# Kernel tuning notes

Hardware: AMD Instinct MI355X
Metric: run time of the kernel (lower is better)

Reference implementation:

```python
import jax, jax.numpy as jnp
import numpy as np

LEAKY_SLOPE = 0.2
DENSITY = 0.05


def setup_inputs() -> dict:
    key = jax.random.key(0)
    k1, k2, k3, k4, k5, k6 = jax.random.split(key, 6)
    N, F_in, F_out = 8192, 128, 64
    h = jax.random.normal(k1, (N, F_in), dtype=jnp.float32)
    # Linear(in, out, bias=False) weight is [out, in]
    W = jax.random.normal(k2, (F_out, F_in), dtype=jnp.float32) * (1.0 / np.sqrt(F_in))
    a_left = jax.random.normal(k3, (F_out,), dtype=jnp.float32) * 0.1
    a_right = jax.random.normal(k4, (F_out,), dtype=jnp.float32) * 0.1
    vals = jax.random.uniform(k5, (N, N), dtype=jnp.float32)
    keep = jax.random.uniform(k6, (N, N)) < DENSITY
    adj = jnp.where(keep, vals, 0.0)  # raw adjacency; self-loops added in reference
    return {"h": h, "W": W, "a_left": a_left, "a_right": a_right, "adj": adj}


def reference(h, W, a_left, a_right, adj):
    N = adj.shape[0]
    A = adj + jnp.eye(N, dtype=adj.dtype)          # A = adjacency + I (self-loops)
    mask = jnp.abs(A) > 0                          # valued-mask support
    Wh = h @ W.T                                   # [N, F_out]
    e_left = Wh @ a_left                           # [N]
    e_right = Wh @ a_right                         # [N]
    e = e_left[:, None] + e_right[None, :]         # [N, N] additive scores
    e = jnp.where(e >= 0, e, LEAKY_SLOPE * e)      # LeakyReLU(0.2)
    e = jnp.where(mask, e, -jnp.inf)               # masked_fill(mask==0, -inf)
    attention = jax.nn.softmax(e, axis=1) * A      # valued masking post-softmax
    # dropout p=0.0 -> identity (eval-mode reference)
    return attention @ Wh                          # [N, F_out]
```

## Files before the change

### kernel.cpp

```cpp
#include <hip/hip_runtime.h>
#include <hip/hip_bf16.h>
#include <hip/hip_fp16.h>

#define N    8192
#define FIN  128
#define FOUT 64
#define LEAKY 0.2f
#define CAP  640
#define LOG2E 1.44269504088896340736f

struct alignas(8) Ent { unsigned joff; float w; };

__global__ __launch_bounds__(256) void wh_eLR_kernel(
    const float* __restrict__ h, const float* __restrict__ Wm,
    const float* __restrict__ aL, const float* __restrict__ aR,
    __half* __restrict__ Whh, float* __restrict__ eL2, float* __restrict__ eR2)
{
    __shared__ float sW[FOUT][FIN + 1];
    __shared__ float sh[4][FIN];
    const int t = threadIdx.x;
    const int rbase = blockIdx.x * 4;

    for (int idx = t; idx < FOUT * FIN; idx += 256)
        sW[idx >> 7][idx & 127] = Wm[idx];
    for (int idx = t; idx < 4 * FIN; idx += 256)
        sh[idx >> 7][idx & 127] = h[(size_t)(rbase + (idx >> 7)) * FIN + (idx & 127)];
    __syncthreads();

    const int wv = t >> 6, f = t & 63;
    const int row = rbase + wv;
    float acc = 0.f;
    #pragma unroll 16
    for (int k = 0; k < FIN; ++k) acc += sh[wv][k] * sW[f][k];
    Whh[(size_t)row * FOUT + f] = __float2half_rn(acc);

    float vl = acc * aL[f];
    float vr = acc * aR[f];
    #pragma unroll
    for (int d = 32; d > 0; d >>= 1) {
        vl += __shfl_down(vl, d, 64);
        vr += __shfl_down(vr, d, 64);
    }
    if (f == 0) { eL2[row] = vl * LOG2E; eR2[row] = vr * LOG2E; }
}

__global__ __launch_bounds__(256) void gat_row_kernel(
    const float* __restrict__ adj, const __half* __restrict__ Whh,
    const float* __restrict__ eL2p, const float* __restrict__ eR2p,
    float* __restrict__ out)
{
    __shared__ Ent ent[4][CAP];
    const int t = threadIdx.x;
    const int wv = t >> 6;
    const int lane = t & 63;
    const int row = blockIdx.x * 4 + wv;

    const float el = eL2p[row];
    const float4* __restrict__ arow4 = (const float4*)(adj + (size_t)row * N);
    const char* __restrict__ er2b = (const char*)eR2p;
    const char* __restrict__ whb  = (const char*)Whh;
    Ent* __restrict__ myent = ent[wv];

    const unsigned l7 = ((unsigned)lane * 4) << 7;
    const unsigned l7u[4] = {l7, l7 + 128, l7 + 256, l7 + 384};
    const unsigned row7 = ((unsigned)row) << 7;
    const int rc = row >> 8;

    const int g  = lane >> 4;
    const int fb = (lane & 15) * 8;

    int base = 0, cs = 0;
    float psum = 0.f;
    float a0x = 0.f, a0y = 0.f, a0z = 0.f, a0w = 0.f;
    float a1x = 0.f, a1y = 0.f, a1z = 0.f, a1w = 0.f;

    float4 b0 = arow4[lane];
    float4 b1 = arow4[64 + lane];

    for (int ch = 0; ch < 16; ++ch) {
        float4 n0, n1;
        if (ch < 15) {
            n0 = arow4[(2 * ch + 2) * 64 + lane];
            n1 = arow4[(2 * ch + 3) * 64 + lane];
        }

        #pragma unroll
        for (int cc = 0; cc < 2; ++cc) {
            const int c = 2 * ch + cc;
            const float4 a4 = cc ? b1 : b0;
            const float av[4] = {a4.x, a4.y, a4.z, a4.w};
            const unsigned cbits = ((unsigned)c) << 15;
            const bool cdiag = (c == rc);
            #pragma unroll
            for (int u = 0; u < 4; ++u) {
                float a = av[u];
                if (cdiag) {
                    if ((cbits | l7u[u]) == row7) a += 1.0f;
                }
                const bool nz = (a != 0.f);
                const unsigned long long m = __ballot(nz);
                const int before = __builtin_amdgcn_mbcnt_hi(
                    (unsigned)(m >> 32),
                    __builtin_amdgcn_mbcnt_lo((unsigned)m, 0));
                if (nz) {
                    Ent e; e.joff = cbits | l7u[u]; e.w = a;
                    myent[base + before] = e;
                }
                base += (int)__popcll(m);
            }
        }

        asm volatile("s_waitcnt lgkmcnt(0)" ::: "memory");

        const int ce = base;
        for (int k = cs + g; k < ce; k += 8) {
            const Ent e0 = myent[k];
            const float er0 = *(const float*)(er2b + (e0.joff >> 5));
            float y0 = el + er0;
            y0 = fmaxf(y0, LEAKY * y0);
            const float p0 = exp2f(y0);
            const uint2 u0 = *(const uint2*)(whb + (e0.joff + fb));
            const float2 f00 = __half22float2(*(const __half2*)&u0.x);
            const float2 f01 = __half22float2(*(const __half2*)&u0.y);
            const float w0 = p0 * e0.w;
            a0x += w0 * f00.x; a0y += w0 * f00.y;
            a0z += w0 * f01.x; a0w += w0 * f01.y;
            psum += p0;
            const int k2 = k + 4;
            if (k2 < ce) {
                const Ent e1 = myent[k2];
                const float er1 = *(const float*)(er2b + (e1.joff >> 5));
                float y1 = el + er1;
                y1 = fmaxf(y1, LEAKY * y1);
                const float p1 = exp2f(y1);
                const uint2 u1 = *(const uint2*)(whb + (e1.joff + fb));
                const float2 f10 = __half22float2(*(const __half2*)&u1.x);
                const float2 f11 = __half22float2(*(const __half2*)&u1.y);
                const float w1 = p1 * e1.w;
                a1x += w1 * f10.x; a1y += w1 * f10.y;
                a1z += w1 * f11.x; a1w += w1 * f11.y;
                psum += p1;
            }
        }
        cs = ce;
        if (ch < 15) { b0 = n0; b1 = n1; }
    }

    float tot = psum;
    tot += __shfl_xor(tot, 16, 64);
    tot += __shfl_xor(tot, 32, 64);
    const float rz = 1.0f / tot;

    a0x += a1x; a0y += a1y; a0z += a1z; a0w += a1w;
    #pragma unroll
    for (int d = 32; d >= 16; d >>= 1) {
        a0x += __shfl_down(a0x, d, 64);
        a0y += __shfl_down(a0y, d, 64);
        a0z += __shfl_down(a0z, d, 64);
        a0w += __shfl_down(a0w, d, 64);
    }
    if (lane < 16) {
        float4 r;
        r.x = a0x * rz; r.y = a0y * rz; r.z = a0z * rz; r.w = a0w * rz;
        *(float4*)(out + (size_t)row * FOUT + (lane & 15) * 4) = r;
    }
}

extern "C" void kernel_launch(void* const* d_in, const int* in_sizes, int n_in,
                              void* d_out, int out_size, void* d_ws, size_t ws_size,
                              hipStream_t stream) {
    const float* h   = (const float*)d_in[0];
    const float* Wm  = (const float*)d_in[1];
    const float* aL  = (const float*)d_in[2];
    const float* aR  = (const float*)d_in[3];
    const float* adj = (const float*)d_in[4];
    float* outp = (float*)d_out;

    __half* Whh = (__half*)d_ws;
    float* eL2  = (float*)((char*)d_ws + (size_t)N * FOUT * 2);
    float* eR2  = eL2 + N;

    wh_eLR_kernel<<<N / 4, 256, 0, stream>>>(h, Wm, aL, aR, Whh, eL2, eR2);
    gat_row_kernel<<<N / 4, 256, 0, stream>>>(adj, Whh, eL2, eR2, outp);
}
```

Baseline: 89.32 us.

## Split each adjacency row across four waves with two rows per block

```diff
diff --git a/kernel.cpp b/kernel.cpp
--- a/kernel.cpp
+++ b/kernel.cpp
@@ -6,7 +6,7 @@
 #define FIN  128
 #define FOUT 64
 #define LEAKY 0.2f
-#define CAP  640
+#define CAPQ 256
 #define LOG2E 1.44269504088896340736f
 
 struct alignas(8) Ent { unsigned joff; float w; };
@@ -44,126 +44,159 @@
     if (f == 0) { eL2[row] = vl * LOG2E; eR2[row] = vr * LOG2E; }
 }
 
-__global__ __launch_bounds__(256) void gat_row_kernel(
+__global__ __launch_bounds__(256, 4) void gat_row_kernel(
     const float* __restrict__ adj, const __half* __restrict__ Whh,
     const float* __restrict__ eL2p, const float* __restrict__ eR2p,
     float* __restrict__ out)
 {
-    __shared__ Ent ent[4][CAP];
+    __shared__ Ent ent[2][4][CAPQ];
+    __shared__ float4 facc[2][4][16];
+    __shared__ float fpsum[2][4];
+
     const int t = threadIdx.x;
     const int wv = t >> 6;
     const int lane = t & 63;
-    const int row = blockIdx.x * 4 + wv;
-
-    const float el = eL2p[row];
-    const float4* __restrict__ arow4 = (const float4*)(adj + (size_t)row * N);
+    const int r0 = blockIdx.x * 2;
+
+    const float el0 = eL2p[r0];
+    const float el1 = eL2p[r0 + 1];
+    const float4* __restrict__ arow0 = (const float4*)(adj + (size_t)r0 * N);
+    const float4* __restrict__ arow1 = (const float4*)(adj + (size_t)(r0 + 1) * N);
     const char* __restrict__ er2b = (const char*)eR2p;
     const char* __restrict__ whb  = (const char*)Whh;
-    Ent* __restrict__ myent = ent[wv];
-
-    const unsigned l7 = ((unsigned)lane * 4) << 7;
+
+    const unsigned l7 = ((unsigned)((wv << 11) + lane * 4)) << 7;
     const unsigned l7u[4] = {l7, l7 + 128, l7 + 256, l7 + 384};
-    const unsigned row7 = ((unsigned)row) << 7;
-    const int rc = row >> 8;
-
     const int g  = lane >> 4;
     const int fb = (lane & 15) * 8;
-
-    int base = 0, cs = 0;
-    float psum = 0.f;
-    float a0x = 0.f, a0y = 0.f, a0z = 0.f, a0w = 0.f;
-    float a1x = 0.f, a1y = 0.f, a1z = 0.f, a1w = 0.f;
-
-    float4 b0 = arow4[lane];
-    float4 b1 = arow4[64 + lane];
-
-    for (int ch = 0; ch < 16; ++ch) {
-        float4 n0, n1;
-        if (ch < 15) {
-            n0 = arow4[(2 * ch + 2) * 64 + lane];
-            n1 = arow4[(2 * ch + 3) * 64 + lane];
-        }
-
-        #pragma unroll
-        for (int cc = 0; cc < 2; ++cc) {
-            const int c = 2 * ch + cc;
-            const float4 a4 = cc ? b1 : b0;
-            const float av[4] = {a4.x, a4.y, a4.z, a4.w};
-            const unsigned cbits = ((unsigned)c) << 15;
-            const bool cdiag = (c == rc);
-            #pragma unroll
-            for (int u = 0; u < 4; ++u) {
-                float a = av[u];
-                if (cdiag) {
-                    if ((cbits | l7u[u]) == row7) a += 1.0f;
-                }
-                const bool nz = (a != 0.f);
-                const unsigned long long m = __ballot(nz);
-                const int before = __builtin_amdgcn_mbcnt_hi(
-                    (unsigned)(m >> 32),
-                    __builtin_amdgcn_mbcnt_lo((unsigned)m, 0));
-                if (nz) {
-                    Ent e; e.joff = cbits | l7u[u]; e.w = a;
-                    myent[base + before] = e;
-                }
-                base += (int)__popcll(m);
-            }
-        }
-
-        asm volatile("s_waitcnt lgkmcnt(0)" ::: "memory");
-
-        const int ce = base;
-        for (int k = cs + g; k < ce; k += 8) {
-            const Ent e0 = myent[k];
-            const float er0 = *(const float*)(er2b + (e0.joff >> 5));
-            float y0 = el + er0;
-            y0 = fmaxf(y0, LEAKY * y0);
-            const float p0 = exp2f(y0);
-            const uint2 u0 = *(const uint2*)(whb + (e0.joff + fb));
-            const float2 f00 = __half22float2(*(const __half2*)&u0.x);
-            const float2 f01 = __half22float2(*(const __half2*)&u0.y);
-            const float w0 = p0 * e0.w;
-            a0x += w0 * f00.x; a0y += w0 * f00.y;
-            a0z += w0 * f01.x; a0w += w0 * f01.y;
-            psum += p0;
-            const int k2 = k + 4;
-            if (k2 < ce) {
-                const Ent e1 = myent[k2];
-                const float er1 = *(const float*)(er2b + (e1.joff >> 5));
-                float y1 = el + er1;
-                y1 = fmaxf(y1, LEAKY * y1);
-                const float p1 = exp2f(y1);
-                const uint2 u1 = *(const uint2*)(whb + (e1.joff + fb));
-                const float2 f10 = __half22float2(*(const __half2*)&u1.x);
-                const float2 f11 = __half22float2(*(const __half2*)&u1.y);
-                const float w1 = p1 * e1.w;
-                a1x += w1 * f10.x; a1y += w1 * f10.y;
-                a1z += w1 * f11.x; a1w += w1 * f11.y;
-                psum += p1;
-            }
-        }
-        cs = ce;
-        if (ch < 15) { b0 = n0; b1 = n1; }
-    }
-
-    float tot = psum;
-    tot += __shfl_xor(tot, 16, 64);
-    tot += __shfl_xor(tot, 32, 64);
-    const float rz = 1.0f / tot;
-
-    a0x += a1x; a0y += a1y; a0z += a1z; a0w += a1w;
+    const int qb = (wv << 9) + lane;
+
+#define COMPACT(BUF, RR, BASE)                                                 \
+    {                                                                          \
+        const int row_ = r0 + (RR);                                            \
+        const unsigned row7_ = ((unsigned)row_) << 7;                          \
+        const int rcl_ = (row_ >> 8) - (wv << 3);                              \
+        _Pragma("unroll")                                                      \
+        for (int c = 0; c < 8; ++c) {                                          \
+            const float4 a4 = BUF[c];                                          \
+            const float av_[4] = {a4.x, a4.y, a4.z, a4.w};                     \
+            const unsigned cbits_ = ((unsigned)c) << 15;                       \
+            const bool cdiag_ = (c == rcl_);                                   \
+            _Pragma("unroll")                                                  \
+            for (int u = 0; u < 4; ++u) {                                      \
+                float a = av_[u];                                              \
+                if (cdiag_) { if ((cbits_ + l7u[u]) == row7_) a += 1.0f; }     \
+                const bool nz = (a != 0.f);                                    \
+                const unsigned long long m_ = __ballot(nz);                    \
+                const int before_ = __builtin_amdgcn_mbcnt_hi(                 \
+                    (unsigned)(m_ >> 32),                                      \
+                    __builtin_amdgcn_mbcnt_lo((unsigned)m_, 0));               \
+                if (nz) {                                                      \
+                    Ent e_; e_.joff = cbits_ + l7u[u]; e_.w = a;               \
+                    ent[RR][wv][BASE + before_] = e_;          \
+                }                                                              \
+                BASE += (int)__popcll(m_);                                     \
+            }                                                                  \
+        }                                                                      \
+    }
+
+#define GATHER(RR, BASE, EL)                                                   \
+    {                                                                          \
+        const int cnt_ = min(BASE, CAPQ - 16);                                 \
+        if (lane < 16) { Ent z_; z_.joff = 0; z_.w = 0.f;                      \
+                         ent[RR][wv][cnt_ + lane] = z_; }                      \
+        asm volatile("s_waitcnt lgkmcnt(0)" ::: "memory");                     \
+        float ax = 0.f, ay = 0.f, az = 0.f, aw = 0.f;                          \
+        float bx = 0.f, by = 0.f, bz = 0.f, bw = 0.f;                          \
+        float cx = 0.f, cy = 0.f, cz = 0.f, cw = 0.f;                          \
+        float dx = 0.f, dy = 0.f, dz = 0.f, dw = 0.f;                          \
+        float psum = 0.f;                                                      \
+        const int cnt16_ = (cnt_ + 15) & ~15;                                  \
+        for (int k = g; k < cnt16_; k += 16) {                                 \
+            const Ent e0 = ent[RR][wv][k];              \
+            const Ent e1 = ent[RR][wv][k + 4];                                 \
+            const Ent e2 = ent[RR][wv][k + 8];                                 \
+            const Ent e3 = ent[RR][wv][k + 12];                                \
+            const float er0 = *(const float*)(er2b + (e0.joff >> 5));          \
+            const float er1 = *(const float*)(er2b + (e1.joff >> 5));          \
+            const float er2 = *(const float*)(er2b + (e2.joff >> 5));          \
+            const float er3 = *(const float*)(er2b + (e3.joff >> 5));          \
+            const uint2 u0 = *(const uint2*)(whb + (e0.joff + fb));            \
+            const uint2 u1 = *(const uint2*)(whb + (e1.joff + fb));            \
+            const uint2 u2 = *(const uint2*)(whb + (e2.joff + fb));            \
+            const uint2 u3 = *(const uint2*)(whb + (e3.joff + fb));            \
+            float y0 = (EL) + er0; y0 = fmaxf(y0, LEAKY * y0);                 \
+            float y1 = (EL) + er1; y1 = fmaxf(y1, LEAKY * y1);                 \
+            float y2 = (EL) + er2; y2 = fmaxf(y2, LEAKY * y2);                 \
+            float y3 = (EL) + er3; y3 = fmaxf(y3, LEAKY * y3);                 \
+            const float p0 = exp2f(y0), p1 = exp2f(y1);                        \
+            const float p2 = exp2f(y2), p3 = exp2f(y3);                        \
+            psum += (e0.w != 0.f ? p0 : 0.f) + (e1.w != 0.f ? p1 : 0.f)        \
+                  + (e2.w != 0.f ? p2 : 0.f) + (e3.w != 0.f ? p3 : 0.f);       \
+            const float w0 = p0 * e0.w, w1 = p1 * e1.w;                        \
+            const float w2 = p2 * e2.w, w3 = p3 * e3.w;                        \
+            const float2 f00 = __half22float2(*(const __half2*)&u0.x);         \
+            const float2 f01 = __half22float2(*(const __half2*)&u0.y);         \
+            const float2 f10 = __half22float2(*(const __half2*)&u1.x);         \
+            const float2 f11 = __half22float2(*(const __half2*)&u1.y);         \
+            const float2 f20 = __half22float2(*(const __half2*)&u2.x);         \
+            const float2 f21 = __half22float2(*(const __half2*)&u2.y);         \
+            const float2 f30 = __half22float2(*(const __half2*)&u3.x);         \
+            const float2 f31 = __half22float2(*(const __half2*)&u3.y);         \
+            ax += w0 * f00.x; ay += w0 * f00.y; az += w0 * f01.x; aw += w0 * f01.y; \
+            bx += w1 * f10.x; by += w1 * f10.y; bz += w1 * f11.x; bw += w1 * f11.y; \
+            cx += w2 * f20.x; cy += w2 * f20.y; cz += w2 * f21.x; cw += w2 * f21.y; \
+            dx += w3 * f30.x; dy += w3 * f30.y; dz += w3 * f31.x; dw += w3 * f31.y; \
+        }                                                                      \
+        ax += bx; ay += by; az += bz; aw += bw;                                \
+        cx += dx; cy += dy; cz += dz; cw += dw;                                \
+        ax += cx; ay += cy; az += cz; aw += cw;                                \
+        _Pragma("unroll")                                                      \
+        for (int d = 32; d >= 16; d >>= 1) {                                   \
+            ax += __shfl_down(ax, d, 64);                                      \
+            ay += __shfl_down(ay, d, 64);                                      \
+            az += __shfl_down(az, d, 64);                                      \
+            aw += __shfl_down(aw, d, 64);                                      \
+            psum += __shfl_down(psum, d, 64);                                  \
+        }                                                                      \
+        if (lane < 16) { float4 p_; p_.x = ax; p_.y = ay; p_.z = az; p_.w = aw; \
+                         facc[RR][wv][lane] = p_; }                            \
+        if (lane == 0) fpsum[RR][wv] = psum;                                   \
+    }
+
+    int base0 = 0, base1 = 0;
+
+    float4 b0[8];
     #pragma unroll
-    for (int d = 32; d >= 16; d >>= 1) {
-        a0x += __shfl_down(a0x, d, 64);
-        a0y += __shfl_down(a0y, d, 64);
-        a0z += __shfl_down(a0z, d, 64);
-        a0w += __shfl_down(a0w, d, 64);
-    }
-    if (lane < 16) {
+    for (int c = 0; c < 8; ++c) b0[c] = arow0[qb + c * 64];
+    COMPACT(b0, 0, base0)
+
+    float4 b1[8];
+    #pragma unroll
+    for (int c = 0; c < 8; ++c) b1[c] = arow1[qb + c * 64];
+
+    GATHER(0, base0, el0)
+    COMPACT(b1, 1, base1)
+    GATHER(1, base1, el1)
+
+    __syncthreads();
+
+    if (wv < 2 && lane < 16) {
+        const float Z = fpsum[wv][0] + fpsum[wv][1] + fpsum[wv][2] + fpsum[wv][3];
+        const float rz = 1.0f / Z;
+        const float4 q0 = facc[wv][0][lane];
+        const float4 q1 = facc[wv][1][lane];
+        const float4 q2 = facc[wv][2][lane];
+        const float4 q3 = facc[wv][3][lane];
         float4 r;
-        r.x = a0x * rz; r.y = a0y * rz; r.z = a0z * rz; r.w = a0w * rz;
-        *(float4*)(out + (size_t)row * FOUT + (lane & 15) * 4) = r;
-    }
+        r.x = (q0.x + q1.x + q2.x + q3.x) * rz;
+        r.y = (q0.y + q1.y + q2.y + q3.y) * rz;
+        r.z = (q0.z + q1.z + q2.z + q3.z) * rz;
+        r.w = (q0.w + q1.w + q2.w + q3.w) * rz;
+        *(float4*)(out + (size_t)(r0 + wv) * FOUT + lane * 4) = r;
+    }
+#undef COMPACT
+#undef GATHER
 }
 
 extern "C" void kernel_launch(void* const* d_in, const int* in_sizes, int n_in,
@@ -181,5 +214,5 @@
     float* eR2  = eL2 + N;
 
     wh_eLR_kernel<<<N / 4, 256, 0, stream>>>(h, Wm, aL, aR, Whh, eL2, eR2);
-    gat_row_kernel<<<N / 4, 256, 0, stream>>>(adj, Whh, eL2, eR2, outp);
+    gat_row_kernel<<<N / 2, 256, 0, stream>>>(adj, Whh, eL2, eR2, outp);
 }
```

After: 89.55 us. About the same (+0.3%).
